# Performance work log

Hardware: AMD Instinct MI355X
Metric: run time of the kernel (lower is better)

Reference implementation:

```python
import jax, jax.numpy as jnp
import numpy as np

D_ATT = 256
D_GROUP = 32
N_GROUP = D_ATT // D_GROUP


def setup_inputs() -> dict:
    key = jax.random.key(0)
    ks = jax.random.split(key, 6)
    B, L = 4, 512
    import math
    s = 1.0 / math.sqrt(D_ATT)
    return {
        "x": jax.random.normal(ks[0], (B, L, D_ATT), dtype=jnp.float32),
        "Wq": jax.random.normal(ks[1], (D_ATT, D_ATT), dtype=jnp.float32) * s * 0.06,
        "Wk": jax.random.normal(ks[2], (D_ATT, D_ATT), dtype=jnp.float32) * s * 0.06,
        "Wv": jax.random.normal(ks[3], (D_ATT, D_ATT), dtype=jnp.float32) * s * 0.06,
        "w_mlp": jax.random.normal(ks[4], (D_GROUP,), dtype=jnp.float32) * 0.1,
        "b_mlp": jax.random.normal(ks[5], (1,), dtype=jnp.float32) * 0.1,
    }


def reference(x, Wq, Wk, Wv, w_mlp, b_mlp):
    B, L, d_att = x.shape
    G, Dg = N_GROUP, D_GROUP
    # nn.Linear(bias=False): y = x @ W.T
    Q = x @ Wq.T  # (B, L, d_att)
    K = x @ Wk.T
    V = x @ Wv.T
    Qg = Q.reshape(B, L, 1, G, Dg)
    Kg = K.reshape(B, 1, L, G, Dg)
    # group_MLP: ReLU -> Linear(Dg, 1) -> ReLU, applied to Q-K diff
    # diff: (B, Lq, Lk, G, Dg) -- the huge intermediate a fused kernel would avoid
    diff = Qg - Kg
    attn = jnp.einsum('bqkgd,d->bqkg', jax.nn.relu(diff), w_mlp) + b_mlp[0]
    attn = jax.nn.relu(attn)
    # positional_adding_bias=0, positional_multiplying_bias=1 (defaults), no mask
    attn = jax.nn.softmax(attn, axis=2)  # softmax over key positions
    # NOTE: original views V as (B, L, d_group, n_group) -- asymmetric grouping, kept faithful
    Vg = V.reshape(B, L, Dg, G)
    out = jnp.einsum('bqkg,bkdg->bqdg', attn, Vg)  # (B, Lq, Dg, G)
    return out.reshape(B, L, d_att)
```

## Files before the change

### kernel.cpp

```cpp
#include <hip/hip_runtime.h>

typedef float f32x2 __attribute__((ext_vector_type(2)));
typedef float f32x4 __attribute__((ext_vector_type(4)));
typedef _Float16 h16x2 __attribute__((ext_vector_type(2)));
typedef _Float16 h16x4 __attribute__((ext_vector_type(4)));
typedef _Float16 h16x8 __attribute__((ext_vector_type(8)));

#define LL 512
#define M_ROWS 2048

#if __has_builtin(__builtin_amdgcn_exp2f)
#define EXP2F __builtin_amdgcn_exp2f
#else
#define EXP2F exp2f
#endif
#define LOG2E 1.44269504088896340736f

__device__ __forceinline__ float quad_swap1(float x) {
    return __int_as_float(__builtin_amdgcn_mov_dpp(__float_as_int(x), 0xB1, 0xF, 0xF, true));
}
__device__ __forceinline__ float quad_swap2(float x) {
    return __int_as_float(__builtin_amdgcn_mov_dpp(__float_as_int(x), 0x4E, 0xF, 0xF, true));
}

__device__ __forceinline__ float fdot2f(h16x2 a, h16x2 b, float c) {
#if __has_builtin(__builtin_amdgcn_fdot2)
    return __builtin_amdgcn_fdot2(a, b, c, false);
#else
    return fmaf((float)a.x, (float)b.x, fmaf((float)a.y, (float)b.y, c));
#endif
}

__global__ __launch_bounds__(128) void qkv_gemm(
    const float* __restrict__ X, const float* __restrict__ Wq,
    const float* __restrict__ Wk, const float* __restrict__ Wv,
    _Float16* __restrict__ Qh, _Float16* __restrict__ Kh, float* __restrict__ Vt)
{
    const int bx = blockIdx.x;
    const int by = blockIdx.y;
    const int mat = bx >> 2;
    const int n0 = (bx & 3) * 64;
    const int m0 = by * 32;
    const float* W = (mat == 0) ? Wq : (mat == 1 ? Wk : Wv);

    __shared__ float As[2][32][36];
    __shared__ float Bs[2][32][68];

    const int t = threadIdx.x;
    const int tx = t & 15;
    const int ty = t >> 4;

    int am[2], ak4[2];
#pragma unroll
    for (int r = 0; r < 2; ++r) { int idx = t + 128 * r; am[r] = idx >> 3; ak4[r] = idx & 7; }
    int bn[4], bk4[4]; size_t brow[4];
#pragma unroll
    for (int r = 0; r < 4; ++r) {
        int idx = t + 128 * r; bn[r] = idx >> 3; bk4[r] = idx & 7;
        int rowc = n0 + bn[r];
        brow[r] = (mat == 2) ? (size_t)(((rowc & 31) << 3) | (rowc >> 5)) : (size_t)rowc;
    }

    f32x4 arg[2], brg[4];
    auto load_tile = [&](int kc) {
#pragma unroll
        for (int r = 0; r < 2; ++r)
            arg[r] = *(const f32x4*)(X + (size_t)(m0 + am[r]) * 256 + kc + ak4[r] * 4);
#pragma unroll
        for (int r = 0; r < 4; ++r)
            brg[r] = *(const f32x4*)(W + brow[r] * 256 + kc + bk4[r] * 4);
    };
    auto store_tile = [&](int buf) {
#pragma unroll
        for (int r = 0; r < 2; ++r)
#pragma unroll
            for (int j = 0; j < 4; ++j) As[buf][ak4[r] * 4 + j][am[r]] = arg[r][j];
#pragma unroll
        for (int r = 0; r < 4; ++r)
#pragma unroll
            for (int j = 0; j < 4; ++j) Bs[buf][bk4[r] * 4 + j][bn[r]] = brg[r][j];
    };

    load_tile(0);
    store_tile(0);
    __syncthreads();

    f32x2 c[4][2];
#pragma unroll
    for (int i = 0; i < 4; ++i) { c[i][0] = (f32x2){0.f, 0.f}; c[i][1] = (f32x2){0.f, 0.f}; }

    for (int it = 0; it < 8; ++it) {
        const int buf = it & 1;
        if (it < 7) load_tile((it + 1) * 32);
#pragma unroll
        for (int kk = 0; kk < 32; ++kk) {
            const f32x4 a4 = *(const f32x4*)&As[buf][kk][ty * 4];
            const f32x4 b4 = *(const f32x4*)&Bs[buf][kk][tx * 4];
            const f32x2 bl = __builtin_shufflevector(b4, b4, 0, 1);
            const f32x2 bh = __builtin_shufflevector(b4, b4, 2, 3);
#pragma unroll
            for (int i = 0; i < 4; ++i) {
                const f32x2 ai = {a4[i], a4[i]};
                c[i][0] += ai * bl;
                c[i][1] += ai * bh;
            }
        }
        if (it < 7) {
            __syncthreads();
            store_tile(buf ^ 1);
            __syncthreads();
        }
    }

    const int colb = n0 + tx * 4;
    if (mat == 2) {
#pragma unroll
        for (int i = 0; i < 4; ++i) {
            f32x4 v = {c[i][0].x, c[i][0].y, c[i][1].x, c[i][1].y};
            *(f32x4*)(Vt + (size_t)(m0 + ty * 4 + i) * 256 + colb) = v;
        }
    } else {
        _Float16* Hb = (mat == 0) ? Qh : Kh;
#pragma unroll
        for (int i = 0; i < 4; ++i) {
            h16x4 hv = {(_Float16)c[i][0].x, (_Float16)c[i][0].y,
                        (_Float16)c[i][1].x, (_Float16)c[i][1].y};
            *(h16x4*)(Hb + (size_t)(m0 + ty * 4 + i) * 256 + colb) = hv;
        }
    }
}

__global__ __launch_bounds__(512, 4) void attn_fused(
    const _Float16* __restrict__ Qh, const _Float16* __restrict__ Kh,
    const float* __restrict__ Vt,
    const float* __restrict__ w_mlp, const float* __restrict__ b_mlp,
    float* __restrict__ out)
{
    const int bid = blockIdx.x;
    const int b = bid & 3;
    const int q0 = (bid >> 2) * 4;

    const int t = threadIdx.x;
    const int dh = t & 3;
    const int p = t >> 5;
    const int lane32 = t & 31;
    const int g = lane32 >> 2;

    __shared__ float accbuf[16][32][19];

    const int doff = g * 32 + dh * 8;
    const float bias4 = b_mlp[0] * (LOG2E * 0.25f);
    const bool odd = (dh & 1) != 0;
    const bool hi  = (dh & 2) != 0;

    h16x2 w2[4];
    {
        f32x4 wa = *(const f32x4*)(w_mlp + dh * 8);
        f32x4 wb = *(const f32x4*)(w_mlp + dh * 8 + 4);
        wa *= LOG2E; wb *= LOG2E;
        w2[0] = (h16x2){(_Float16)wa.x, (_Float16)wa.y};
        w2[1] = (h16x2){(_Float16)wa.z, (_Float16)wa.w};
        w2[2] = (h16x2){(_Float16)wb.x, (_Float16)wb.y};
        w2[3] = (h16x2){(_Float16)wb.z, (_Float16)wb.w};
    }

    h16x2 qr2[4][4];
#pragma unroll
    for (int q = 0; q < 4; ++q) {
        const h16x8 qv = *(const h16x8*)(Qh + ((size_t)(b * LL) + q0 + q) * 256 + doff);
        qr2[q][0] = __builtin_shufflevector(qv, qv, 0, 1);
        qr2[q][1] = __builtin_shufflevector(qv, qv, 2, 3);
        qr2[q][2] = __builtin_shufflevector(qv, qv, 4, 5);
        qr2[q][3] = __builtin_shufflevector(qv, qv, 6, 7);
    }

    f32x2 acc2[4][4];
#pragma unroll
    for (int s = 0; s < 4; ++s)
#pragma unroll
        for (int j = 0; j < 4; ++j) acc2[s][j] = (f32x2){0.f, 0.f};
    float lown = 0.f;

    const _Float16* kptr = Kh + ((size_t)(b * LL) + p) * 256 + doff;
    const float* vptr = Vt + ((size_t)(b * LL) + p) * 256 + doff;

    const h16x2 zh = {(_Float16)0.f, (_Float16)0.f};

    auto compute = [&](h16x8 kv, f32x4 va, f32x4 vb) {
        h16x2 k2[4] = {__builtin_shufflevector(kv, kv, 0, 1),
                       __builtin_shufflevector(kv, kv, 2, 3),
                       __builtin_shufflevector(kv, kv, 4, 5),
                       __builtin_shufflevector(kv, kv, 6, 7)};
        f32x2 v2[4] = {__builtin_shufflevector(va, va, 0, 1),
                       __builtin_shufflevector(va, va, 2, 3),
                       __builtin_shufflevector(vb, vb, 0, 1),
                       __builtin_shufflevector(vb, vb, 2, 3)};
        float ps[4];
#pragma unroll
        for (int q = 0; q < 4; ++q) {
            float s = bias4;
#pragma unroll
            for (int j = 0; j < 4; ++j) {
                h16x2 d2 = qr2[q][j] - k2[j];
                h16x2 r2 = __builtin_elementwise_max(d2, zh);
                s = fdot2f(w2[j], r2, s);
            }
            ps[q] = s;
        }
        const float r01 = quad_swap1(odd ? ps[0] : ps[1]);
        const float z01 = (odd ? ps[1] : ps[0]) + r01;
        const float r23 = quad_swap1(odd ? ps[2] : ps[3]);
        const float z23 = (odd ? ps[3] : ps[2]) + r23;
        const float r2f = quad_swap2(hi ? z01 : z23);
        const float zz  = (hi ? z23 : z01) + r2f;
        const float sfull = fmaxf(zz, 0.f);
        const float e = EXP2F(sfull);
        lown += e;
        const float e1 = quad_swap1(e);
        const float e2 = quad_swap2(e);
        const float e3 = quad_swap2(e1);
        const float es[4] = {e, e1, e2, e3};
#pragma unroll
        for (int s = 0; s < 4; ++s) {
            const f32x2 ee = {es[s], es[s]};
#pragma unroll
            for (int j = 0; j < 4; ++j)
                acc2[s][j] = __builtin_elementwise_fma(v2[j], ee, acc2[s][j]);
        }
    };

    h16x8 kc = *(const h16x8*)kptr;
    f32x4 va = *(const f32x4*)vptr, vb = *(const f32x4*)(vptr + 4);
#pragma unroll 1
    for (int i = 0; i < 31; ++i) {
        kptr += 16 * 256; vptr += 16 * 256;
        h16x8 kn = *(const h16x8*)kptr;
        f32x4 va2 = *(const f32x4*)vptr, vb2 = *(const f32x4*)(vptr + 4);
        compute(kc, va, vb);
        kc = kn; va = va2; vb = vb2;
    }
    compute(kc, va, vb);

    const int c_o = t & 255;
    const int g_o = c_o & 7, d_o = c_o >> 3;
    const int rowb = g_o * 4 + (d_o >> 3);
    const int colb = d_o & 7;
    const int qh2 = t >> 8;

#pragma unroll
    for (int r = 0; r < 2; ++r) {
        if (r) __syncthreads();
        {
            float* rowp = &accbuf[p][lane32][0];
#pragma unroll
            for (int s = 0; s < 4; ++s) {
                const int qq = dh ^ s;
                if ((qq >> 1) == r) {
#pragma unroll
                    for (int j = 0; j < 4; ++j)
                        *(f32x2*)(rowp + (qq & 1) * 8 + j * 2) = acc2[s][j];
                }
            }
            if ((dh >> 1) == r) rowp[16 + (dh & 1)] = lown;
        }
        __syncthreads();
        {
            const int q = 2 * r + qh2;
            float s = 0.f, ls = 0.f;
#pragma unroll
            for (int pp = 0; pp < 16; ++pp) {
                s  += accbuf[pp][rowb][qh2 * 8 + colb];
                ls += accbuf[pp][g_o * 4 + q][16 + qh2];
            }
            out[((size_t)(b * LL) + q0 + q) * 256 + c_o] = s / ls;
        }
    }
}

extern "C" void kernel_launch(void* const* d_in, const int* in_sizes, int n_in,
                              void* d_out, int out_size, void* d_ws, size_t ws_size,
                              hipStream_t stream) {
    (void)in_sizes; (void)n_in; (void)out_size; (void)ws_size;
    const float* x     = (const float*)d_in[0];
    const float* Wq    = (const float*)d_in[1];
    const float* Wk    = (const float*)d_in[2];
    const float* Wv    = (const float*)d_in[3];
    const float* w_mlp = (const float*)d_in[4];
    const float* b_mlp = (const float*)d_in[5];
    float* outp = (float*)d_out;

    _Float16* Qh = (_Float16*)d_ws;
    _Float16* Kh = (_Float16*)((char*)d_ws + (size_t)1048576);
    float*    Vt = (float*)((char*)d_ws + (size_t)2097152);

    qkv_gemm<<<dim3(12, 64), 128, 0, stream>>>(x, Wq, Wk, Wv, Qh, Kh, Vt);
    attn_fused<<<dim3(512), 512, 0, stream>>>(Qh, Kh, Vt, w_mlp, b_mlp, outp);
}
```

Baseline: 108.6 us.

## Process eight queries per 1024-thread block so wave halves share K/V loads

Doubles the attention block to 1024 threads covering eight query rows, with key partitions indexed per 64-lane wave. The two 32-lane halves of each wave now handle different query quads against the same K/V rows, halving K/V global loads per query. The final cross-partition reduction is rewritten to write all accumulators to a larger LDS buffer in one pass, with a single barrier. In exchange, LDS use grows to about 139KB per block and the grid shrinks to 256 blocks, leaving one block per CU and less latency hiding across blocks.

```diff
diff --git a/kernel.cpp b/kernel.cpp
--- a/kernel.cpp
+++ b/kernel.cpp
@@ -130,7 +130,7 @@
     }
 }
 
-__global__ __launch_bounds__(512, 4) void attn_fused(
+__global__ __launch_bounds__(1024, 4) void attn_fused(
     const _Float16* __restrict__ Qh, const _Float16* __restrict__ Kh,
     const float* __restrict__ Vt,
     const float* __restrict__ w_mlp, const float* __restrict__ b_mlp,
@@ -138,15 +138,17 @@
 {
     const int bid = blockIdx.x;
     const int b = bid & 3;
-    const int q0 = (bid >> 2) * 4;
+    const int q0 = (bid >> 2) * 8;
 
     const int t = threadIdx.x;
+    const int p = t >> 6;
+    const int lane64 = t & 63;
+    const int half = (t >> 5) & 1;
+    const int lane32 = t & 31;
     const int dh = t & 3;
-    const int p = t >> 5;
-    const int lane32 = t & 31;
     const int g = lane32 >> 2;
 
-    __shared__ float accbuf[16][32][19];
+    __shared__ float accbuf[16][64][34];
 
     const int doff = g * 32 + dh * 8;
     const float bias4 = b_mlp[0] * (LOG2E * 0.25f);
@@ -167,7 +169,7 @@
     h16x2 qr2[4][4];
 #pragma unroll
     for (int q = 0; q < 4; ++q) {
-        const h16x8 qv = *(const h16x8*)(Qh + ((size_t)(b * LL) + q0 + q) * 256 + doff);
+        const h16x8 qv = *(const h16x8*)(Qh + ((size_t)(b * LL) + q0 + half * 4 + q) * 256 + doff);
         qr2[q][0] = __builtin_shufflevector(qv, qv, 0, 1);
         qr2[q][1] = __builtin_shufflevector(qv, qv, 2, 3);
         qr2[q][2] = __builtin_shufflevector(qv, qv, 4, 5);
@@ -241,39 +243,36 @@
     }
     compute(kc, va, vb);
 
-    const int c_o = t & 255;
-    const int g_o = c_o & 7, d_o = c_o >> 3;
-    const int rowb = g_o * 4 + (d_o >> 3);
-    const int colb = d_o & 7;
-    const int qh2 = t >> 8;
+    {
+        float* rowp = &accbuf[p][lane64][0];
+#pragma unroll
+        for (int s = 0; s < 4; ++s)
+#pragma unroll
+            for (int j = 0; j < 4; ++j)
+                *(f32x2*)(rowp + s * 8 + j * 2) = acc2[s][j];
+        rowp[32] = lown;
+    }
+    __syncthreads();
 
 #pragma unroll
     for (int r = 0; r < 2; ++r) {
-        if (r) __syncthreads();
-        {
-            float* rowp = &accbuf[p][lane32][0];
-#pragma unroll
-            for (int s = 0; s < 4; ++s) {
-                const int qq = dh ^ s;
-                if ((qq >> 1) == r) {
-#pragma unroll
-                    for (int j = 0; j < 4; ++j)
-                        *(f32x2*)(rowp + (qq & 1) * 8 + j * 2) = acc2[s][j];
-                }
-            }
-            if ((dh >> 1) == r) rowp[16 + (dh & 1)] = lown;
-        }
-        __syncthreads();
-        {
-            const int q = 2 * r + qh2;
-            float s = 0.f, ls = 0.f;
-#pragma unroll
-            for (int pp = 0; pp < 16; ++pp) {
-                s  += accbuf[pp][rowb][qh2 * 8 + colb];
-                ls += accbuf[pp][g_o * 4 + q][16 + qh2];
-            }
-            out[((size_t)(b * LL) + q0 + q) * 256 + c_o] = s / ls;
-        }
+        const int o = t + 1024 * r;
+        const int q = o >> 8;
+        const int c = o & 255;
+        const int gs = c & 7;
+        const int dd = c >> 3;
+        const int dhs = dd >> 3;
+        const int rem = dd & 7;
+        const int s = dhs ^ (q & 3);
+        const int lsrc = (q >> 2) * 32 + gs * 4 + dhs;
+        const int lden = (q >> 2) * 32 + gs * 4 + (q & 3);
+        float sum = 0.f, den = 0.f;
+#pragma unroll
+        for (int pp = 0; pp < 16; ++pp) {
+            sum += accbuf[pp][lsrc][s * 8 + rem];
+            den += accbuf[pp][lden][32];
+        }
+        out[((size_t)(b * LL) + q0 + q) * 256 + c] = sum / den;
     }
 }
 
@@ -294,5 +293,5 @@
     float*    Vt = (float*)((char*)d_ws + (size_t)2097152);
 
     qkv_gemm<<<dim3(12, 64), 128, 0, stream>>>(x, Wq, Wk, Wv, Qh, Kh, Vt);
-    attn_fused<<<dim3(512), 512, 0, stream>>>(Qh, Kh, Vt, w_mlp, b_mlp, outp);
-}
+    attn_fused<<<dim3(256), 1024, 0, stream>>>(Qh, Kh, Vt, w_mlp, b_mlp, outp);
+}
```

New measurement: 110.1 us. Within noise of the previous version (+1.4%).
